# Kernel tuning notes

Hardware: AMD Instinct MI355X
Metric: run time of the kernel (lower is better)

## Reference

```python
import jax, jax.numpy as jnp
import numpy as np
from jax import lax

B, C, L = 2048, 9605, 8
WL_PER_LABEL = 50
ALPHA = 0.5        # training_config['alpha4']
ALPHA1 = 0.1       # margin
ALPHA2 = 2.0       # training_config['alpha2']
ALPHA3 = 10.0      # training_config['alpha3']
ALPHA_OTHER = 0.5
NEG = jnp.float32(-1e30)


def setup_inputs() -> dict:
    key = jax.random.key(0)
    k1, k2, k3, k4 = jax.random.split(key, 4)
    x = jax.random.normal(k1, (B, C), dtype=jnp.float32) * 2.0
    y = (jax.random.uniform(k2, (B, C)) < 0.005).astype(jnp.float32)
    y_neg = (jax.random.uniform(k3, (B, C)) < 0.005).astype(jnp.float32)
    # whitelist masks: L app-labels, each whitelisting ~WL_PER_LABEL raw classes
    idx = jax.random.randint(k4, (L, WL_PER_LABEL), 0, C)
    wl_masks = jnp.zeros((L, C), dtype=bool).at[jnp.arange(L)[:, None], idx].set(True)
    return {"x": x, "y": y, "y_neg": y_neg, "wl_masks": wl_masks}


def reference(x, y, y_neg, wl_masks):
    # y_neg is consumed by the original forward (find_gt_whitelist) but never
    # affects the returned loss, faithfully ignored here.
    xs_pos = jax.nn.sigmoid(x)                                  # [B, C]
    # top_k_thres = max(11th-largest sigmoid, alpha_other)
    thres = jnp.maximum(lax.top_k(xs_pos, 11)[0][:, 10], ALPHA_OTHER)  # [B]
    # per-label whitelist max: m[b,l] = max_{c in wl_l} xs_pos[b,c]
    m = jnp.max(jnp.where(wl_masks[None, :, :], xs_pos[:, None, :], NEG), axis=-1)  # [B, L]
    # label l is a ground-truth whitelist label iff y has any positive in wl_l
    has_pos = jnp.einsum('bc,lc->bl', y, wl_masks.astype(y.dtype)) > 0   # [B, L]
    correct_max = jnp.max(jnp.where(has_pos, m, NEG), axis=-1)           # [B]
    incorrect_max = jnp.max(jnp.where(~has_pos, m, NEG), axis=-1)        # [B]
    any_correct = jnp.any(has_pos, axis=-1)
    any_incorrect = jnp.any(~has_pos, axis=-1)
    # union whitelist max (the "other" branch uses xs_pos over all wl indices)
    union_max = jnp.max(jnp.where(jnp.any(wl_masks, axis=0)[None, :], xs_pos, NEG), axis=-1)
    x1 = jnp.where(any_correct, correct_max, thres)
    x2 = jnp.where(any_correct,
                   jnp.where(any_incorrect, jnp.maximum(incorrect_max, thres), thres),
                   union_max)
    coef = jnp.where(any_correct, 1.0, 1.0 - ALPHA)
    d = x2 - x1 + ALPHA1
    rank = jnp.where(d > 0, ALPHA2, 1.0) * jax.nn.sigmoid(ALPHA3 * d)
    return jnp.mean(coef * rank)
```

## Files before the change

### kernel.cpp

```cpp
#include <hip/hip_runtime.h>

#define CC 9605
#define BB 2048
#define LL 8
#define CAND_MAX 384
#define NEGF (-1e30f)

#define WS_PARTIALS_OFF 16384

__device__ __forceinline__ unsigned enc_f(float f) {
  unsigned u = __float_as_uint(f);
  return (u & 0x80000000u) ? ~u : (u | 0x80000000u);
}
__device__ __forceinline__ float dec_u(unsigned e) {
  unsigned u = (e & 0x80000000u) ? (e & 0x7fffffffu) : ~e;
  return __uint_as_float(u);
}
__device__ __forceinline__ float sigm(float z) {
  return 1.0f / (1.0f + __expf(-z));
}
__device__ __forceinline__ unsigned prefix_lt(unsigned long long m) {
  unsigned r = __builtin_amdgcn_mbcnt_lo((unsigned)m, 0u);
  return __builtin_amdgcn_mbcnt_hi((unsigned)(m >> 32), r);
}

__global__ void wl_sniff(const unsigned* __restrict__ wlw,
                         unsigned* __restrict__ wsu) {
  const int nwords = (LL * CC) / 4;
  const int stride = gridDim.x * blockDim.x;
  unsigned f = 0u;
  for (int j = blockIdx.x * blockDim.x + threadIdx.x; j < nwords; j += stride) {
    unsigned w = wlw[j];
#pragma unroll
    for (int k = 0; k < 4; ++k) {
      unsigned b = (w >> (8 * k)) & 255u;
      if (b == 1u)    { f |= 2u; if (k != 0) f |= 1u; }
      if (b == 0x3fu) { f |= 8u; if (k == 1) f |= 4u; }
    }
  }
#pragma unroll
  for (int off = 32; off >= 1; off >>= 1) f |= __shfl_xor(f, off, 64);
  if ((threadIdx.x & 63) == 0 && f) atomicOr(&wsu[1], f);
}

__global__ void wl_compact(const unsigned char* __restrict__ wl,
                           unsigned* __restrict__ wsu) {
  const int tid = threadIdx.x;
  const int lane = tid & 63;
  const int c = blockIdx.x * 256 + tid;
  const unsigned g = wsu[1];
  const int dt = (g & 1u) ? 0 : (g & 4u) ? 3 : (g & 2u) ? 1 : (g & 8u) ? 2 : 0;
  const int* wl32 = (const int*)wl;
  const float* wlf = (const float*)wl;
  const unsigned short* wlh = (const unsigned short*)wl;
  unsigned m = 0u;
  if (c < CC) {
#pragma unroll
    for (int l = 0; l < LL; ++l) {
      int j = l * CC + c;
      bool on;
      if (dt == 0) on = (wl[j] != 0);
      else if (dt == 1) on = (wl32[j] != 0);
      else if (dt == 2) on = (wlf[j] != 0.0f);
      else on = (wlh[j] != 0);
      if (on) m |= (1u << l);
    }
  }
  unsigned long long bal = __ballot(m != 0u);
  if (bal) {
    unsigned wcnt = (unsigned)__popcll(bal);
    unsigned basep = 0u;
    if (lane == 0) basep = atomicAdd(&wsu[0], wcnt);
    basep = __shfl(basep, 0, 64);
    if (m) {
      unsigned pos = basep + (unsigned)__popcll(bal & ((1ull << lane) - 1ull));
      if (pos < 2048u) wsu[4 + pos] = ((unsigned)c << 8) | m;
    }
  }
}


#define ENCMAX(U, T)                                            \
  do {                                                          \
    U.x = enc_f(T.x); U.y = enc_f(T.y);                         \
    U.z = enc_f(T.z); U.w = enc_f(T.w);                         \
    mx = max(mx, max(max(U.x, U.y), max(U.z, U.w)));            \
  } while (0)

#define CNT4(U, T)                                              \
  (((U.x >= (T)) ? 1u : 0u) + ((U.y >= (T)) ? 1u : 0u) +        \
   ((U.z >= (T)) ? 1u : 0u) + ((U.w >= (T)) ? 1u : 0u))

#define BLK_COUNT(T, RES)                                       \
  do {                                                          \
    unsigned _c = CNT4(u0, (T)) + CNT4(u1, (T)) + CNT4(u2, (T)) \
                + CNT4(u3, (T)) + CNT4(u4, (T))                 \
                + ((et >= (T)) ? 1u : 0u);                      \
    unsigned _w = (unsigned)__popcll(__ballot(_c & 1u));        \
    _w += (unsigned)__popcll(__ballot(_c & 2u)) << 1;           \
    _w += (unsigned)__popcll(__ballot(_c & 4u)) << 2;           \
    _w += (unsigned)__popcll(__ballot(_c & 8u)) << 3;           \
    _w += (unsigned)__popcll(__ballot(_c & 16u)) << 4;          \
    __syncthreads();                   \
    if (lane == 0) sh_redC[wid] = _w;                           \
    __syncthreads();                                            \
    RES = sh_redC[0] + sh_redC[1] + sh_redC[2] + sh_redC[3] +   \
          sh_redC[4] + sh_redC[5] + sh_redC[6] + sh_redC[7];    \
  } while (0)

#define EMIT(V)                                                 \
  do {                                                          \
    if ((V) >= lo) sh_cand[pos++] = (V);                        \
  } while (0)

__global__ __launch_bounds__(512) void loss_kernel(
    const float* __restrict__ x, const float* __restrict__ y,
    const unsigned* __restrict__ wsu, float* __restrict__ partials) {
  __shared__ unsigned sh_cand[CAND_MAX];
  __shared__ unsigned sh_redM[8];
  __shared__ unsigned sh_redC[8];
  __shared__ unsigned sh_cnt;
  __shared__ float sh_wl[8][10];

  const int tid = threadIdx.x;
  const int lane = tid & 63;
  const int wid = tid >> 6;
  const int b = blockIdx.x;
  const long long base = (long long)b * CC;

  const int soff = (4 - (b & 3)) & 3;
  const int ngroups = (CC - soff) >> 2;
  const int tailn = CC - soff - (ngroups << 2);
  const int m_extra = soff + tailn;
  const float4* vp = (const float4*)(x + base + soff);
  float4 t0 = vp[tid];
  float4 t1 = vp[tid + 512];
  float4 t2 = vp[tid + 1024];
  float4 t3 = vp[tid + 1536];
  const int g4 = tid + 2048;
  const bool v4 = (g4 < ngroups);
  float4 t4 = make_float4(0.0f, 0.0f, 0.0f, 0.0f);
  if (v4) t4 = vp[g4];
  float tailv = 0.0f;
  const bool has_tail = (tid < m_extra);
  if (has_tail) {
    int tailcol = (tid < soff) ? tid : (soff + (ngroups << 2) + (tid - soff));
    tailv = x[base + tailcol];
  }

  const unsigned nu = min(wsu[0], 2048u);
  const unsigned* ents = wsu + 4;
  unsigned ent0 = 0u;
  float gx0 = NEGF, gy0 = 0.0f;
  const bool h0 = (unsigned)tid < nu;
  if (h0) ent0 = ents[tid];
  if (h0) { gx0 = x[base + (ent0 >> 8)]; gy0 = y[base + (ent0 >> 8)]; }

  unsigned mx = 0u;
  uint4 u0, u1, u2, u3, u4;
  ENCMAX(u0, t0);
  ENCMAX(u1, t1);
  ENCMAX(u2, t2);
  ENCMAX(u3, t3);
  if (v4) {
    ENCMAX(u4, t4);
  } else {
    u4.x = 0u; u4.y = 0u; u4.z = 0u; u4.w = 0u;
  }
  unsigned et = 0u;
  if (has_tail) { et = enc_f(tailv); mx = max(mx, et); }
  if (tid == 0) sh_cnt = 0u;

  mx = max(mx, __shfl_xor(mx, 32, 64));
  mx = max(mx, __shfl_xor(mx, 16, 64));
  mx = max(mx, __shfl_xor(mx, 8, 64));
  mx = max(mx, __shfl_xor(mx, 4, 64));
  mx = max(mx, __shfl_xor(mx, 2, 64));
  mx = max(mx, __shfl_xor(mx, 1, 64));
  if (lane == 0) sh_redM[wid] = mx;
  __syncthreads();
  unsigned Emax = sh_redM[0];
#pragma unroll
  for (int w = 1; w < 8; ++w) Emax = max(Emax, sh_redM[w]);

  unsigned E11 = 0u;
  bool done = false;
  unsigned lo = (Emax > (1u << 23)) ? (Emax - (1u << 23)) : 1u;
  unsigned hi = Emax + 1u;
  unsigned c;
  BLK_COUNT(lo, c);
  while (c < 11u && lo > 1u) {
    hi = lo;
    lo = (lo > (1u << 23)) ? (lo - (1u << 23)) : 1u;
    BLK_COUNT(lo, c);
  }
  while (c > CAND_MAX) {
    if (hi - lo <= 1u) { E11 = lo; done = true; break; }
    unsigned mid = lo + ((hi - lo) >> 1);
    unsigned cm;
    BLK_COUNT(mid, cm);
    if (cm >= 11u) { lo = mid; c = cm; } else { hi = mid; }
  }

  if (!done) {
    unsigned nloc = CNT4(u0, lo) + CNT4(u1, lo) + CNT4(u2, lo) +
                    CNT4(u3, lo) + CNT4(u4, lo) + ((et >= lo) ? 1u : 0u);
    unsigned long long m0 = __ballot(nloc & 1u);
    unsigned long long m1 = __ballot(nloc & 2u);
    unsigned long long m2 = __ballot(nloc & 4u);
    unsigned long long m3 = __ballot(nloc & 8u);
    unsigned long long m4 = __ballot(nloc & 16u);
    unsigned wtot = (unsigned)__popcll(m0) + ((unsigned)__popcll(m1) << 1) +
                    ((unsigned)__popcll(m2) << 2) +
                    ((unsigned)__popcll(m3) << 3) +
                    ((unsigned)__popcll(m4) << 4);
    unsigned pre = prefix_lt(m0) + (prefix_lt(m1) << 1) +
                   (prefix_lt(m2) << 2) + (prefix_lt(m3) << 3) +
                   (prefix_lt(m4) << 4);
    unsigned basep = 0u;
    if (lane == 0) basep = atomicAdd(&sh_cnt, wtot);
    basep = (unsigned)__builtin_amdgcn_readfirstlane((int)basep);
    unsigned pos = basep + pre;
    EMIT(u0.x); EMIT(u0.y); EMIT(u0.z); EMIT(u0.w);
    EMIT(u1.x); EMIT(u1.y); EMIT(u1.z); EMIT(u1.w);
    EMIT(u2.x); EMIT(u2.y); EMIT(u2.z); EMIT(u2.w);
    EMIT(u3.x); EMIT(u3.y); EMIT(u3.z); EMIT(u3.w);
    EMIT(u4.x); EMIT(u4.y); EMIT(u4.z); EMIT(u4.w);
    EMIT(et);
    __syncthreads();
  }

  {
    float lm[8];
#pragma unroll
    for (int l = 0; l < 8; ++l) lm[l] = NEGF;
    unsigned pmask = 0u;
    if (h0) {
      unsigned mk = ent0 & 255u;
      pmask |= mk;
      if (gy0 > 0.0f) pmask |= (mk << 8);
#pragma unroll
      for (int l = 0; l < 8; ++l)
        if ((mk >> l) & 1u) lm[l] = fmaxf(lm[l], gx0);
    }
    for (unsigned e = (unsigned)tid + 512u; e < nu; e += 512u) {
      unsigned ent = ents[e];
      unsigned mk = ent & 255u;
      float xv = x[base + (ent >> 8)];
      float yv = y[base + (ent >> 8)];
      pmask |= mk;
      if (yv > 0.0f) pmask |= (mk << 8);
#pragma unroll
      for (int l = 0; l < 8; ++l)
        if ((mk >> l) & 1u) lm[l] = fmaxf(lm[l], xv);
    }
#pragma unroll
    for (int off = 32; off >= 1; off >>= 1) {
      pmask |= __shfl_xor(pmask, off, 64);
#pragma unroll
      for (int l = 0; l < 8; ++l)
        lm[l] = fmaxf(lm[l], __shfl_xor(lm[l], off, 64));
    }
    if (lane == 0) {
#pragma unroll
      for (int l = 0; l < 8; ++l) sh_wl[wid][l] = lm[l];
      sh_wl[wid][8] = __uint_as_float(pmask);
    }
  }

  if (!done && wid == 0) {
    unsigned c0 = ((unsigned)lane < c) ? sh_cand[lane] : 0u;
    unsigned c1 = ((unsigned)lane + 64u < c) ? sh_cand[lane + 64u] : 0u;
    unsigned c2 = ((unsigned)lane + 128u < c) ? sh_cand[lane + 128u] : 0u;
    unsigned c3 = ((unsigned)lane + 192u < c) ? sh_cand[lane + 192u] : 0u;
    unsigned c4 = ((unsigned)lane + 256u < c) ? sh_cand[lane + 256u] : 0u;
    unsigned c5 = ((unsigned)lane + 320u < c) ? sh_cand[lane + 320u] : 0u;
    unsigned blo = lo, bhi = hi;
    while (bhi - blo > 1u) {
      unsigned mid = blo + ((bhi - blo) >> 1);
      unsigned cnt = (unsigned)__popcll(__ballot(c0 >= mid)) +
                     (unsigned)__popcll(__ballot(c1 >= mid)) +
                     (unsigned)__popcll(__ballot(c2 >= mid)) +
                     (unsigned)__popcll(__ballot(c3 >= mid)) +
                     (unsigned)__popcll(__ballot(c4 >= mid)) +
                     (unsigned)__popcll(__ballot(c5 >= mid));
      if (cnt >= 11u) blo = mid; else bhi = mid;
    }
    E11 = blo;
  }
  __syncthreads();

  if (tid == 0) {
    float LM[8];
    unsigned PM = 0u;
#pragma unroll
    for (int l = 0; l < 8; ++l) LM[l] = NEGF;
    for (int w = 0; w < 8; ++w) {
#pragma unroll
      for (int l = 0; l < 8; ++l) LM[l] = fmaxf(LM[l], sh_wl[w][l]);
      PM |= __float_as_uint(sh_wl[w][8]);
    }
    unsigned PR = PM & 255u, PO = (PM >> 8) & 255u;
    float thres = fmaxf(sigm(dec_u(E11)), 0.5f);
    float cmax = NEGF, imax = NEGF, umax = NEGF;
#pragma unroll
    for (int l = 0; l < 8; ++l) {
      if ((PR >> l) & 1u) {
        float ml = sigm(LM[l]);
        umax = fmaxf(umax, ml);
        if ((PO >> l) & 1u) cmax = fmaxf(cmax, ml);
        else imax = fmaxf(imax, ml);
      }
    }
    bool anyc = (PO != 0u);
    bool anyi = (PO != 255u);
    float x1 = anyc ? cmax : thres;
    float x2 = anyc ? (anyi ? fmaxf(imax, thres) : thres)
                    : ((nu > 0u) ? umax : NEGF);
    float coef = anyc ? 1.0f : 0.5f;
    float dd = x2 - x1 + 0.1f;
    float rank = ((dd > 0.0f) ? 2.0f : 1.0f) * sigm(10.0f * dd);
    partials[b] = coef * rank;
  }
}

__global__ void final_reduce(const float* __restrict__ partials,
                             float* __restrict__ out) {
  __shared__ float sh[4];
  const int tid = threadIdx.x;
  const int lane = tid & 63;
  const int wid = tid >> 6;
  float s = 0.0f;
  for (int i = tid; i < BB; i += 256) s += partials[i];
#pragma unroll
  for (int off = 32; off >= 1; off >>= 1) s += __shfl_xor(s, off, 64);
  if (lane == 0) sh[wid] = s;
  __syncthreads();
  if (tid == 0) out[0] = (sh[0] + sh[1] + sh[2] + sh[3]) * (1.0f / (float)BB);
}

extern "C" void kernel_launch(void* const* d_in, const int* in_sizes, int n_in,
                              void* d_out, int out_size, void* d_ws,
                              size_t ws_size, hipStream_t stream) {
  const float* x = (const float*)d_in[0];
  const float* y = (const float*)d_in[1];
  const unsigned char* wl = (const unsigned char*)d_in[3];
  float* out = (float*)d_out;
  unsigned* wsu = (unsigned*)d_ws;
  float* partials = (float*)((char*)d_ws + WS_PARTIALS_OFF);

  hipMemsetAsync(d_ws, 0, 16, stream);
  wl_sniff<<<64, 256, 0, stream>>>((const unsigned*)wl, wsu);
  wl_compact<<<(CC + 255) / 256, 256, 0, stream>>>(wl, wsu);
  loss_kernel<<<BB, 512, 0, stream>>>(x, y, wsu, partials);
  final_reduce<<<1, 256, 0, stream>>>(partials, out);
}
```

Baseline: 220.6 us.

## Process four rows per block with double-buffered register prefetch of next row

Launches 512 persistent-style blocks that each handle four rows, loading the next row's x values into a second register set while the current row is processed, so global load latency overlaps the selection and reduction work. It also replaces __syncthreads with a custom barrier that only waits on LDS counters, so in-flight global prefetches are not drained at each barrier. Register pressure roughly doubles, and the launch bound is set to 4 blocks per CU, which risks spills or lower occupancy. There is also a possible hazard: the shared buffers are reused between rows without an explicit barrier at row start.

```diff
diff --git a/kernel.cpp b/kernel.cpp
--- a/kernel.cpp
+++ b/kernel.cpp
@@ -5,6 +5,8 @@
 #define LL 8
 #define CAND_MAX 384
 #define NEGF (-1e30f)
+#define NBLK 512
+#define ROWSPB (BB / NBLK)
 
 #define WS_PARTIALS_OFF 16384
 
@@ -22,6 +24,12 @@
 __device__ __forceinline__ unsigned prefix_lt(unsigned long long m) {
   unsigned r = __builtin_amdgcn_mbcnt_lo((unsigned)m, 0u);
   return __builtin_amdgcn_mbcnt_hi((unsigned)(m >> 32), r);
+}
+__device__ __forceinline__ void syncb() {
+  __builtin_amdgcn_sched_barrier(0);
+  asm volatile("s_waitcnt lgkmcnt(0)" ::: "memory");
+  __builtin_amdgcn_s_barrier();
+  __builtin_amdgcn_sched_barrier(0);
 }
 
 __global__ void wl_sniff(const unsigned* __restrict__ wlw,
@@ -79,7 +87,6 @@
   }
 }
 
-
 #define ENCMAX(U, T)                                            \
   do {                                                          \
     U.x = enc_f(T.x); U.y = enc_f(T.y);                         \
@@ -101,9 +108,9 @@
     _w += (unsigned)__popcll(__ballot(_c & 4u)) << 2;           \
     _w += (unsigned)__popcll(__ballot(_c & 8u)) << 3;           \
     _w += (unsigned)__popcll(__ballot(_c & 16u)) << 4;          \
-    __syncthreads();                   \
+    syncb();                           \
     if (lane == 0) sh_redC[wid] = _w;                           \
-    __syncthreads();                                            \
+    syncb();                                                    \
     RES = sh_redC[0] + sh_redC[1] + sh_redC[2] + sh_redC[3] +   \
           sh_redC[4] + sh_redC[5] + sh_redC[6] + sh_redC[7];    \
   } while (0)
@@ -113,48 +120,16 @@
     if ((V) >= lo) sh_cand[pos++] = (V);                        \
   } while (0)
 
-__global__ __launch_bounds__(512) void loss_kernel(
+__device__ __forceinline__ void process_row(
     const float* __restrict__ x, const float* __restrict__ y,
-    const unsigned* __restrict__ wsu, float* __restrict__ partials) {
-  __shared__ unsigned sh_cand[CAND_MAX];
-  __shared__ unsigned sh_redM[8];
-  __shared__ unsigned sh_redC[8];
-  __shared__ unsigned sh_cnt;
-  __shared__ float sh_wl[8][10];
-
-  const int tid = threadIdx.x;
-  const int lane = tid & 63;
-  const int wid = tid >> 6;
-  const int b = blockIdx.x;
-  const long long base = (long long)b * CC;
-
-  const int soff = (4 - (b & 3)) & 3;
-  const int ngroups = (CC - soff) >> 2;
-  const int tailn = CC - soff - (ngroups << 2);
-  const int m_extra = soff + tailn;
-  const float4* vp = (const float4*)(x + base + soff);
-  float4 t0 = vp[tid];
-  float4 t1 = vp[tid + 512];
-  float4 t2 = vp[tid + 1024];
-  float4 t3 = vp[tid + 1536];
-  const int g4 = tid + 2048;
-  const bool v4 = (g4 < ngroups);
-  float4 t4 = make_float4(0.0f, 0.0f, 0.0f, 0.0f);
-  if (v4) t4 = vp[g4];
-  float tailv = 0.0f;
-  const bool has_tail = (tid < m_extra);
-  if (has_tail) {
-    int tailcol = (tid < soff) ? tid : (soff + (ngroups << 2) + (tid - soff));
-    tailv = x[base + tailcol];
-  }
-
-  const unsigned nu = min(wsu[0], 2048u);
-  const unsigned* ents = wsu + 4;
-  unsigned ent0 = 0u;
-  float gx0 = NEGF, gy0 = 0.0f;
-  const bool h0 = (unsigned)tid < nu;
-  if (h0) ent0 = ents[tid];
-  if (h0) { gx0 = x[base + (ent0 >> 8)]; gy0 = y[base + (ent0 >> 8)]; }
+    const unsigned* __restrict__ ents, unsigned nu, int r,
+    int tid, int lane, int wid,
+    float4 t0, float4 t1, float4 t2, float4 t3, float4 t4,
+    bool v4, bool ht, float tv, float gx, float gy,
+    bool h0, unsigned mk0,
+    unsigned* sh_cand, unsigned* sh_redM, unsigned* sh_redC,
+    unsigned* sh_cnt, float (*sh_wl)[10], float* __restrict__ partials) {
+  const long long base = (long long)r * CC;
 
   unsigned mx = 0u;
   uint4 u0, u1, u2, u3, u4;
@@ -168,8 +143,8 @@
     u4.x = 0u; u4.y = 0u; u4.z = 0u; u4.w = 0u;
   }
   unsigned et = 0u;
-  if (has_tail) { et = enc_f(tailv); mx = max(mx, et); }
-  if (tid == 0) sh_cnt = 0u;
+  if (ht) { et = enc_f(tv); mx = max(mx, et); }
+  if (tid == 0) *sh_cnt = 0u;
 
   mx = max(mx, __shfl_xor(mx, 32, 64));
   mx = max(mx, __shfl_xor(mx, 16, 64));
@@ -178,7 +153,7 @@
   mx = max(mx, __shfl_xor(mx, 2, 64));
   mx = max(mx, __shfl_xor(mx, 1, 64));
   if (lane == 0) sh_redM[wid] = mx;
-  __syncthreads();
+  syncb();
   unsigned Emax = sh_redM[0];
 #pragma unroll
   for (int w = 1; w < 8; ++w) Emax = max(Emax, sh_redM[w]);
@@ -218,7 +193,7 @@
                    (prefix_lt(m2) << 2) + (prefix_lt(m3) << 3) +
                    (prefix_lt(m4) << 4);
     unsigned basep = 0u;
-    if (lane == 0) basep = atomicAdd(&sh_cnt, wtot);
+    if (lane == 0) basep = atomicAdd(sh_cnt, wtot);
     basep = (unsigned)__builtin_amdgcn_readfirstlane((int)basep);
     unsigned pos = basep + pre;
     EMIT(u0.x); EMIT(u0.y); EMIT(u0.z); EMIT(u0.w);
@@ -227,7 +202,7 @@
     EMIT(u3.x); EMIT(u3.y); EMIT(u3.z); EMIT(u3.w);
     EMIT(u4.x); EMIT(u4.y); EMIT(u4.z); EMIT(u4.w);
     EMIT(et);
-    __syncthreads();
+    syncb();
   }
 
   {
@@ -236,12 +211,11 @@
     for (int l = 0; l < 8; ++l) lm[l] = NEGF;
     unsigned pmask = 0u;
     if (h0) {
-      unsigned mk = ent0 & 255u;
-      pmask |= mk;
-      if (gy0 > 0.0f) pmask |= (mk << 8);
+      pmask |= mk0;
+      if (gy > 0.0f) pmask |= (mk0 << 8);
 #pragma unroll
       for (int l = 0; l < 8; ++l)
-        if ((mk >> l) & 1u) lm[l] = fmaxf(lm[l], gx0);
+        if ((mk0 >> l) & 1u) lm[l] = fmaxf(lm[l], gx);
     }
     for (unsigned e = (unsigned)tid + 512u; e < nu; e += 512u) {
       unsigned ent = ents[e];
@@ -288,7 +262,7 @@
     }
     E11 = blo;
   }
-  __syncthreads();
+  syncb();
 
   if (tid == 0) {
     float LM[8];
@@ -320,8 +294,78 @@
     float coef = anyc ? 1.0f : 0.5f;
     float dd = x2 - x1 + 0.1f;
     float rank = ((dd > 0.0f) ? 2.0f : 1.0f) * sigm(10.0f * dd);
-    partials[b] = coef * rank;
-  }
+    partials[r] = coef * rank;
+  }
+}
+
+#define LOADROW(S, R)                                                     \
+  do {                                                                    \
+    const int _r = (R);                                                   \
+    const long long _base = (long long)_r * CC;                           \
+    const int _soff = (4 - (_r & 3)) & 3;                                 \
+    const int _ng = (CC - _soff) >> 2;                                    \
+    const int _me = CC - (_ng << 2);               \
+    const float4* _vp = (const float4*)(x + _base + _soff);               \
+    t##S##0 = _vp[tid];                                                   \
+    t##S##1 = _vp[tid + 512];                                             \
+    t##S##2 = _vp[tid + 1024];                                            \
+    t##S##3 = _vp[tid + 1536];                                            \
+    v4##S = (tid + 2048 < _ng);                                           \
+    if (v4##S) t##S##4 = _vp[tid + 2048];                                 \
+    ht##S = (tid < _me);                                                  \
+    if (ht##S) {                                                          \
+      int _tc = (tid < _soff) ? tid                                       \
+                              : (_soff + (_ng << 2) + (tid - _soff));     \
+      tv##S = x[_base + _tc];                                             \
+    }                                                                     \
+    if (h0) { gx##S = x[_base + wlcol]; gy##S = y[_base + wlcol]; }       \
+  } while (0)
+
+__global__ __launch_bounds__(512, 4) void loss_kernel(
+    const float* __restrict__ x, const float* __restrict__ y,
+    const unsigned* __restrict__ wsu, float* __restrict__ partials) {
+  __shared__ unsigned sh_cand[CAND_MAX];
+  __shared__ unsigned sh_redM[8];
+  __shared__ unsigned sh_redC[8];
+  __shared__ unsigned sh_cnt;
+  __shared__ float sh_wl[8][10];
+
+  const int tid = threadIdx.x;
+  const int lane = tid & 63;
+  const int wid = tid >> 6;
+  const int bid = blockIdx.x;
+
+  const unsigned nu = min(wsu[0], 2048u);
+  const unsigned* ents = wsu + 4;
+  const bool h0 = (unsigned)tid < nu;
+  unsigned ent0 = 0u;
+  if (h0) ent0 = ents[tid];
+  const int wlcol = (int)(ent0 >> 8);
+  const unsigned mk0 = ent0 & 255u;
+
+  float4 tA0, tA1, tA2, tA3, tA4 = make_float4(0.f, 0.f, 0.f, 0.f);
+  float4 tB0, tB1, tB2, tB3, tB4 = make_float4(0.f, 0.f, 0.f, 0.f);
+  bool v4A = false, htA = false, v4B = false, htB = false;
+  float tvA = 0.f, gxA = NEGF, gyA = 0.f;
+  float tvB = 0.f, gxB = NEGF, gyB = 0.f;
+
+  const int r0 = bid;
+  LOADROW(A, r0);
+  LOADROW(B, r0 + NBLK);
+  process_row(x, y, ents, nu, r0, tid, lane, wid,
+              tA0, tA1, tA2, tA3, tA4, v4A, htA, tvA, gxA, gyA,
+              h0, mk0, sh_cand, sh_redM, sh_redC, &sh_cnt, sh_wl, partials);
+  LOADROW(A, r0 + 2 * NBLK);
+  process_row(x, y, ents, nu, r0 + NBLK, tid, lane, wid,
+              tB0, tB1, tB2, tB3, tB4, v4B, htB, tvB, gxB, gyB,
+              h0, mk0, sh_cand, sh_redM, sh_redC, &sh_cnt, sh_wl, partials);
+  LOADROW(B, r0 + 3 * NBLK);
+  process_row(x, y, ents, nu, r0 + 2 * NBLK, tid, lane, wid,
+              tA0, tA1, tA2, tA3, tA4, v4A, htA, tvA, gxA, gyA,
+              h0, mk0, sh_cand, sh_redM, sh_redC, &sh_cnt, sh_wl, partials);
+  process_row(x, y, ents, nu, r0 + 3 * NBLK, tid, lane, wid,
+              tB0, tB1, tB2, tB3, tB4, v4B, htB, tvB, gxB, gyB,
+              h0, mk0, sh_cand, sh_redM, sh_redC, &sh_cnt, sh_wl, partials);
 }
 
 __global__ void final_reduce(const float* __restrict__ partials,
@@ -352,6 +396,6 @@
   hipMemsetAsync(d_ws, 0, 16, stream);
   wl_sniff<<<64, 256, 0, stream>>>((const unsigned*)wl, wsu);
   wl_compact<<<(CC + 255) / 256, 256, 0, stream>>>(wl, wsu);
-  loss_kernel<<<BB, 512, 0, stream>>>(x, y, wsu, partials);
+  loss_kernel<<<NBLK, 512, 0, stream>>>(x, y, wsu, partials);
   final_reduce<<<1, 256, 0, stream>>>(partials, out);
 }
```

Measured after the change: 233.5 us. 1.06x slower.

## Switch to one wavefront per row with per-lane top-11 insertion sort

Applied to the files above, without the earlier changes.

Restructures the loss kernel so each 64-lane wavefront handles a whole row, four rows per 256-thread block, in place of a 512-thread block per row. Each lane keeps a register sorted top-11 list through a min/max insertion network while streaming the row with double-buffered float4 loads. A wavefront-only binary search over the encoded candidates then finds the 11th largest, which removes block-wide syncthreads, shared-memory candidate compaction and the multi-round block counting. The cost is heavy per-element ALU work (11 min/max pairs per value) and fewer threads per row, which could make the kernel compute-bound.

```diff
diff --git a/kernel.cpp b/kernel.cpp
--- a/kernel.cpp
+++ b/kernel.cpp
@@ -3,8 +3,8 @@
 #define CC 9605
 #define BB 2048
 #define LL 8
-#define CAND_MAX 384
 #define NEGF (-1e30f)
+#define NINF (-__builtin_huge_valf())
 
 #define WS_PARTIALS_OFF 16384
 
@@ -18,10 +18,6 @@
 }
 __device__ __forceinline__ float sigm(float z) {
   return 1.0f / (1.0f + __expf(-z));
-}
-__device__ __forceinline__ unsigned prefix_lt(unsigned long long m) {
-  unsigned r = __builtin_amdgcn_mbcnt_lo((unsigned)m, 0u);
-  return __builtin_amdgcn_mbcnt_hi((unsigned)(m >> 32), r);
 }
 
 __global__ void wl_sniff(const unsigned* __restrict__ wlw,
@@ -80,238 +76,149 @@
 }
 
 
-#define ENCMAX(U, T)                                            \
-  do {                                                          \
-    U.x = enc_f(T.x); U.y = enc_f(T.y);                         \
-    U.z = enc_f(T.z); U.w = enc_f(T.w);                         \
-    mx = max(mx, max(max(U.x, U.y), max(U.z, U.w)));            \
-  } while (0)
-
-#define CNT4(U, T)                                              \
-  (((U.x >= (T)) ? 1u : 0u) + ((U.y >= (T)) ? 1u : 0u) +        \
-   ((U.z >= (T)) ? 1u : 0u) + ((U.w >= (T)) ? 1u : 0u))
-
-#define BLK_COUNT(T, RES)                                       \
-  do {                                                          \
-    unsigned _c = CNT4(u0, (T)) + CNT4(u1, (T)) + CNT4(u2, (T)) \
-                + CNT4(u3, (T)) + CNT4(u4, (T))                 \
-                + ((et >= (T)) ? 1u : 0u);                      \
-    unsigned _w = (unsigned)__popcll(__ballot(_c & 1u));        \
-    _w += (unsigned)__popcll(__ballot(_c & 2u)) << 1;           \
-    _w += (unsigned)__popcll(__ballot(_c & 4u)) << 2;           \
-    _w += (unsigned)__popcll(__ballot(_c & 8u)) << 3;           \
-    _w += (unsigned)__popcll(__ballot(_c & 16u)) << 4;          \
-    __syncthreads();                   \
-    if (lane == 0) sh_redC[wid] = _w;                           \
-    __syncthreads();                                            \
-    RES = sh_redC[0] + sh_redC[1] + sh_redC[2] + sh_redC[3] +   \
-          sh_redC[4] + sh_redC[5] + sh_redC[6] + sh_redC[7];    \
-  } while (0)
-
-#define EMIT(V)                                                 \
-  do {                                                          \
-    if ((V) >= lo) sh_cand[pos++] = (V);                        \
-  } while (0)
-
-__global__ __launch_bounds__(512) void loss_kernel(
+#define FOR11(OP) OP(0) OP(1) OP(2) OP(3) OP(4) OP(5) OP(6) OP(7) OP(8) OP(9) OP(10)
+#define FOR8(OP) OP(0) OP(1) OP(2) OP(3) OP(4) OP(5) OP(6) OP(7)
+
+#define DECL_S(k) float s_##k = NINF;
+#define INS1(k) { float _hi = fmaxf(s_##k, cv); cv = fminf(s_##k, cv); s_##k = _hi; }
+#define TOP11V(v) { float cv = (v); FOR11(INS1) }
+#define TOP4(T) { TOP11V((T).x) TOP11V((T).y) TOP11V((T).z) TOP11V((T).w) }
+
+__global__ __launch_bounds__(256) void loss_kernel(
     const float* __restrict__ x, const float* __restrict__ y,
     const unsigned* __restrict__ wsu, float* __restrict__ partials) {
-  __shared__ unsigned sh_cand[CAND_MAX];
-  __shared__ unsigned sh_redM[8];
-  __shared__ unsigned sh_redC[8];
-  __shared__ unsigned sh_cnt;
-  __shared__ float sh_wl[8][10];
-
   const int tid = threadIdx.x;
   const int lane = tid & 63;
   const int wid = tid >> 6;
-  const int b = blockIdx.x;
-  const long long base = (long long)b * CC;
-
-  const int soff = (4 - (b & 3)) & 3;
-  const int ngroups = (CC - soff) >> 2;
-  const int tailn = CC - soff - (ngroups << 2);
+  const int r = blockIdx.x * 4 + wid;
+  const long long base = (long long)r * CC;
+
+  const unsigned nu = min(wsu[0], 2048u);
+  const unsigned* ents = wsu + 4;
+  unsigned entv[7];
+  float gxv[7], gyv[7];
+#pragma unroll
+  for (int k = 0; k < 7; ++k) {
+    unsigned e = (unsigned)lane + 64u * (unsigned)k;
+    entv[k] = (e < nu) ? ents[e] : 0u;
+  }
+#pragma unroll
+  for (int k = 0; k < 7; ++k) {
+    int col = (int)(entv[k] >> 8);
+    gxv[k] = x[base + col];
+    gyv[k] = y[base + col];
+  }
+
+  const int soff = (4 - (r & 3)) & 3;
+  const int ng = (CC - soff) >> 2;
+  const int rem = ng - 2368;
+  const int tailn = CC - soff - (ng << 2);
   const int m_extra = soff + tailn;
   const float4* vp = (const float4*)(x + base + soff);
-  float4 t0 = vp[tid];
-  float4 t1 = vp[tid + 512];
-  float4 t2 = vp[tid + 1024];
-  float4 t3 = vp[tid + 1536];
-  const int g4 = tid + 2048;
-  const bool v4 = (g4 < ngroups);
-  float4 t4 = make_float4(0.0f, 0.0f, 0.0f, 0.0f);
-  if (v4) t4 = vp[g4];
-  float tailv = 0.0f;
-  const bool has_tail = (tid < m_extra);
-  if (has_tail) {
-    int tailcol = (tid < soff) ? tid : (soff + (ngroups << 2) + (tid - soff));
-    tailv = x[base + tailcol];
-  }
-
-  const unsigned nu = min(wsu[0], 2048u);
-  const unsigned* ents = wsu + 4;
-  unsigned ent0 = 0u;
-  float gx0 = NEGF, gy0 = 0.0f;
-  const bool h0 = (unsigned)tid < nu;
-  if (h0) ent0 = ents[tid];
-  if (h0) { gx0 = x[base + (ent0 >> 8)]; gy0 = y[base + (ent0 >> 8)]; }
-
-  unsigned mx = 0u;
-  uint4 u0, u1, u2, u3, u4;
-  ENCMAX(u0, t0);
-  ENCMAX(u1, t1);
-  ENCMAX(u2, t2);
-  ENCMAX(u3, t3);
-  if (v4) {
-    ENCMAX(u4, t4);
-  } else {
-    u4.x = 0u; u4.y = 0u; u4.z = 0u; u4.w = 0u;
-  }
-  unsigned et = 0u;
-  if (has_tail) { et = enc_f(tailv); mx = max(mx, et); }
-  if (tid == 0) sh_cnt = 0u;
-
-  mx = max(mx, __shfl_xor(mx, 32, 64));
-  mx = max(mx, __shfl_xor(mx, 16, 64));
-  mx = max(mx, __shfl_xor(mx, 8, 64));
-  mx = max(mx, __shfl_xor(mx, 4, 64));
-  mx = max(mx, __shfl_xor(mx, 2, 64));
-  mx = max(mx, __shfl_xor(mx, 1, 64));
-  if (lane == 0) sh_redM[wid] = mx;
-  __syncthreads();
-  unsigned Emax = sh_redM[0];
-#pragma unroll
-  for (int w = 1; w < 8; ++w) Emax = max(Emax, sh_redM[w]);
-
-  unsigned E11 = 0u;
-  bool done = false;
-  unsigned lo = (Emax > (1u << 23)) ? (Emax - (1u << 23)) : 1u;
-  unsigned hi = Emax + 1u;
-  unsigned c;
-  BLK_COUNT(lo, c);
-  while (c < 11u && lo > 1u) {
-    hi = lo;
-    lo = (lo > (1u << 23)) ? (lo - (1u << 23)) : 1u;
-    BLK_COUNT(lo, c);
-  }
-  while (c > CAND_MAX) {
-    if (hi - lo <= 1u) { E11 = lo; done = true; break; }
+
+  FOR11(DECL_S)
+
+  float4 a0 = vp[lane];
+  float4 a1 = vp[lane + 64];
+  float4 a2 = vp[lane + 128];
+  float4 a3 = vp[lane + 192];
+  int gb = lane;
+  for (int i = 0; i + 8 <= 37; i += 4) {
+    float4 b0 = vp[gb + 256];
+    float4 b1 = vp[gb + 320];
+    float4 b2 = vp[gb + 384];
+    float4 b3 = vp[gb + 448];
+    TOP4(a0) TOP4(a1) TOP4(a2) TOP4(a3)
+    a0 = b0; a1 = b1; a2 = b2; a3 = b3;
+    gb += 256;
+  }
+  TOP4(a0) TOP4(a1) TOP4(a2) TOP4(a3)
+  {
+    float4 t = vp[lane + 2304];
+    TOP4(t)
+  }
+  {
+    float4 t = make_float4(NINF, NINF, NINF, NINF);
+    if (lane < rem) t = vp[2368 + lane];
+    TOP4(t)
+  }
+  {
+    float tv = NINF;
+    if (lane < m_extra) {
+      int tc = (lane < soff) ? lane : (soff + (ng << 2) + (lane - soff));
+      tv = x[base + tc];
+    }
+    TOP11V(tv)
+  }
+
+#define DECL_E(k) unsigned e_##k = enc_f(s_##k);
+  FOR11(DECL_E)
+  unsigned wlo = e_10;
+  unsigned whi = e_0;
+#pragma unroll
+  for (int off = 32; off >= 1; off >>= 1) {
+    wlo = max(wlo, __shfl_xor(wlo, off, 64));
+    whi = max(whi, __shfl_xor(whi, off, 64));
+  }
+  unsigned lo = wlo, hi = whi + 1u;
+  while (hi - lo > 1u) {
     unsigned mid = lo + ((hi - lo) >> 1);
-    unsigned cm;
-    BLK_COUNT(mid, cm);
-    if (cm >= 11u) { lo = mid; c = cm; } else { hi = mid; }
-  }
-
-  if (!done) {
-    unsigned nloc = CNT4(u0, lo) + CNT4(u1, lo) + CNT4(u2, lo) +
-                    CNT4(u3, lo) + CNT4(u4, lo) + ((et >= lo) ? 1u : 0u);
-    unsigned long long m0 = __ballot(nloc & 1u);
-    unsigned long long m1 = __ballot(nloc & 2u);
-    unsigned long long m2 = __ballot(nloc & 4u);
-    unsigned long long m3 = __ballot(nloc & 8u);
-    unsigned long long m4 = __ballot(nloc & 16u);
-    unsigned wtot = (unsigned)__popcll(m0) + ((unsigned)__popcll(m1) << 1) +
-                    ((unsigned)__popcll(m2) << 2) +
-                    ((unsigned)__popcll(m3) << 3) +
-                    ((unsigned)__popcll(m4) << 4);
-    unsigned pre = prefix_lt(m0) + (prefix_lt(m1) << 1) +
-                   (prefix_lt(m2) << 2) + (prefix_lt(m3) << 3) +
-                   (prefix_lt(m4) << 4);
-    unsigned basep = 0u;
-    if (lane == 0) basep = atomicAdd(&sh_cnt, wtot);
-    basep = (unsigned)__builtin_amdgcn_readfirstlane((int)basep);
-    unsigned pos = basep + pre;
-    EMIT(u0.x); EMIT(u0.y); EMIT(u0.z); EMIT(u0.w);
-    EMIT(u1.x); EMIT(u1.y); EMIT(u1.z); EMIT(u1.w);
-    EMIT(u2.x); EMIT(u2.y); EMIT(u2.z); EMIT(u2.w);
-    EMIT(u3.x); EMIT(u3.y); EMIT(u3.z); EMIT(u3.w);
-    EMIT(u4.x); EMIT(u4.y); EMIT(u4.z); EMIT(u4.w);
-    EMIT(et);
-    __syncthreads();
-  }
-
-  {
-    float lm[8];
-#pragma unroll
-    for (int l = 0; l < 8; ++l) lm[l] = NEGF;
-    unsigned pmask = 0u;
-    if (h0) {
-      unsigned mk = ent0 & 255u;
-      pmask |= mk;
-      if (gy0 > 0.0f) pmask |= (mk << 8);
-#pragma unroll
-      for (int l = 0; l < 8; ++l)
-        if ((mk >> l) & 1u) lm[l] = fmaxf(lm[l], gx0);
-    }
-    for (unsigned e = (unsigned)tid + 512u; e < nu; e += 512u) {
-      unsigned ent = ents[e];
-      unsigned mk = ent & 255u;
-      float xv = x[base + (ent >> 8)];
-      float yv = y[base + (ent >> 8)];
-      pmask |= mk;
-      if (yv > 0.0f) pmask |= (mk << 8);
-#pragma unroll
-      for (int l = 0; l < 8; ++l)
-        if ((mk >> l) & 1u) lm[l] = fmaxf(lm[l], xv);
-    }
-#pragma unroll
-    for (int off = 32; off >= 1; off >>= 1) {
-      pmask |= __shfl_xor(pmask, off, 64);
-#pragma unroll
-      for (int l = 0; l < 8; ++l)
-        lm[l] = fmaxf(lm[l], __shfl_xor(lm[l], off, 64));
-    }
-    if (lane == 0) {
-#pragma unroll
-      for (int l = 0; l < 8; ++l) sh_wl[wid][l] = lm[l];
-      sh_wl[wid][8] = __uint_as_float(pmask);
-    }
-  }
-
-  if (!done && wid == 0) {
-    unsigned c0 = ((unsigned)lane < c) ? sh_cand[lane] : 0u;
-    unsigned c1 = ((unsigned)lane + 64u < c) ? sh_cand[lane + 64u] : 0u;
-    unsigned c2 = ((unsigned)lane + 128u < c) ? sh_cand[lane + 128u] : 0u;
-    unsigned c3 = ((unsigned)lane + 192u < c) ? sh_cand[lane + 192u] : 0u;
-    unsigned c4 = ((unsigned)lane + 256u < c) ? sh_cand[lane + 256u] : 0u;
-    unsigned c5 = ((unsigned)lane + 320u < c) ? sh_cand[lane + 320u] : 0u;
-    unsigned blo = lo, bhi = hi;
-    while (bhi - blo > 1u) {
-      unsigned mid = blo + ((bhi - blo) >> 1);
-      unsigned cnt = (unsigned)__popcll(__ballot(c0 >= mid)) +
-                     (unsigned)__popcll(__ballot(c1 >= mid)) +
-                     (unsigned)__popcll(__ballot(c2 >= mid)) +
-                     (unsigned)__popcll(__ballot(c3 >= mid)) +
-                     (unsigned)__popcll(__ballot(c4 >= mid)) +
-                     (unsigned)__popcll(__ballot(c5 >= mid));
-      if (cnt >= 11u) blo = mid; else bhi = mid;
-    }
-    E11 = blo;
-  }
-  __syncthreads();
-
-  if (tid == 0) {
-    float LM[8];
-    unsigned PM = 0u;
-#pragma unroll
-    for (int l = 0; l < 8; ++l) LM[l] = NEGF;
-    for (int w = 0; w < 8; ++w) {
-#pragma unroll
-      for (int l = 0; l < 8; ++l) LM[l] = fmaxf(LM[l], sh_wl[w][l]);
-      PM |= __float_as_uint(sh_wl[w][8]);
-    }
-    unsigned PR = PM & 255u, PO = (PM >> 8) & 255u;
+    unsigned cnt = 0u;
+#define CMP1(k) cnt += (e_##k >= mid) ? 1u : 0u;
+    FOR11(CMP1)
+#undef CMP1
+    unsigned tot = (unsigned)__popcll(__ballot(cnt & 1u)) +
+                   ((unsigned)__popcll(__ballot(cnt & 2u)) << 1) +
+                   ((unsigned)__popcll(__ballot(cnt & 4u)) << 2) +
+                   ((unsigned)__popcll(__ballot(cnt & 8u)) << 3);
+    if (tot >= 11u) lo = mid; else hi = mid;
+  }
+  const unsigned E11 = lo;
+
+#define DECL_LM(k) float lm_##k = NEGF;
+  FOR8(DECL_LM)
+  unsigned pmask = 0u;
+#pragma unroll
+  for (int k = 0; k < 7; ++k) {
+    unsigned mk = entv[k] & 255u;
+    pmask |= mk;
+    if (gyv[k] > 0.0f) pmask |= (mk << 8);
+#define FOLD1(l) if ((mk >> l) & 1u) lm_##l = fmaxf(lm_##l, gxv[k]);
+    FOR8(FOLD1)
+#undef FOLD1
+  }
+  for (unsigned e = (unsigned)lane + 448u; e < nu; e += 64u) {
+    unsigned ent = ents[e];
+    unsigned mk = ent & 255u;
+    float xv = x[base + (ent >> 8)];
+    float yv = y[base + (ent >> 8)];
+    pmask |= mk;
+    if (yv > 0.0f) pmask |= (mk << 8);
+#define FOLD1(l) if ((mk >> l) & 1u) lm_##l = fmaxf(lm_##l, xv);
+    FOR8(FOLD1)
+#undef FOLD1
+  }
+#pragma unroll
+  for (int off = 32; off >= 1; off >>= 1) {
+    pmask |= __shfl_xor(pmask, off, 64);
+#define RED1(l) lm_##l = fmaxf(lm_##l, __shfl_xor(lm_##l, off, 64));
+    FOR8(RED1)
+#undef RED1
+  }
+
+  if (lane == 0) {
+    unsigned PR = pmask & 255u, PO = (pmask >> 8) & 255u;
     float thres = fmaxf(sigm(dec_u(E11)), 0.5f);
     float cmax = NEGF, imax = NEGF, umax = NEGF;
-#pragma unroll
-    for (int l = 0; l < 8; ++l) {
-      if ((PR >> l) & 1u) {
-        float ml = sigm(LM[l]);
-        umax = fmaxf(umax, ml);
-        if ((PO >> l) & 1u) cmax = fmaxf(cmax, ml);
-        else imax = fmaxf(imax, ml);
-      }
-    }
+#define EP1(l)                                                   \
+    if ((PR >> l) & 1u) {                                        \
+      float ml = sigm(lm_##l);                                   \
+      umax = fmaxf(umax, ml);                                    \
+      if ((PO >> l) & 1u) cmax = fmaxf(cmax, ml);                \
+      else imax = fmaxf(imax, ml);                               \
+    }
+    FOR8(EP1)
+#undef EP1
     bool anyc = (PO != 0u);
     bool anyi = (PO != 255u);
     float x1 = anyc ? cmax : thres;
@@ -320,7 +227,7 @@
     float coef = anyc ? 1.0f : 0.5f;
     float dd = x2 - x1 + 0.1f;
     float rank = ((dd > 0.0f) ? 2.0f : 1.0f) * sigm(10.0f * dd);
-    partials[b] = coef * rank;
+    partials[r] = coef * rank;
   }
 }
 
@@ -352,6 +259,6 @@
   hipMemsetAsync(d_ws, 0, 16, stream);
   wl_sniff<<<64, 256, 0, stream>>>((const unsigned*)wl, wsu);
   wl_compact<<<(CC + 255) / 256, 256, 0, stream>>>(wl, wsu);
-  loss_kernel<<<BB, 512, 0, stream>>>(x, y, wsu, partials);
+  loss_kernel<<<BB / 4, 256, 0, stream>>>(x, y, wsu, partials);
   final_reduce<<<1, 256, 0, stream>>>(partials, out);
 }
```

After: 234.0 us. 6.1% more time.
